# Kernel optimization log

Hardware: AMD Instinct MI355X
Metric: run time of the kernel (lower is better)

The kernel has to match this reference:

```python
import jax, jax.numpy as jnp
import numpy as np

D_MODEL = 1024
NUM_HEADS = 16
HEAD_DIM = D_MODEL // NUM_HEADS
THETA = 10000.0


def apply_rope(x, token_positions):
    # x: [B, H, S, d_head]; token_positions: [S] int
    d = x.shape[-1]
    inv_freq = THETA ** (-jnp.arange(0, d, 2, dtype=jnp.float32) / d)  # [d/2]
    ang = token_positions.astype(jnp.float32)[:, None] * inv_freq      # [S, d/2]
    cos, sin = jnp.cos(ang), jnp.sin(ang)
    x1 = x[..., 0::2]
    x2 = x[..., 1::2]
    out_even = x1 * cos - x2 * sin
    out_odd = x1 * sin + x2 * cos
    # interleave even/odd back: [..., S, d/2, 2] -> [..., S, d]
    return jnp.stack([out_even, out_odd], axis=-1).reshape(x.shape)


def setup_inputs() -> dict:
    key = jax.random.key(0)
    ks = jax.random.split(key, 5)
    scale = 1.0 / np.sqrt(D_MODEL)
    x = jax.random.normal(ks[0], (4, 2048, D_MODEL), dtype=jnp.float32)
    wq = jax.random.normal(ks[1], (D_MODEL, D_MODEL), dtype=jnp.float32) * scale
    wk = jax.random.normal(ks[2], (D_MODEL, D_MODEL), dtype=jnp.float32) * scale
    wv = jax.random.normal(ks[3], (D_MODEL, D_MODEL), dtype=jnp.float32) * scale
    wo = jax.random.normal(ks[4], (D_MODEL, D_MODEL), dtype=jnp.float32) * scale
    token_positions = jnp.arange(2048, dtype=jnp.int32)
    return {"x": x, "wq": wq, "wk": wk, "wv": wv, "wo": wo,
            "token_positions": token_positions}


def reference(x, wq, wk, wv, wo, token_positions):
    B, S, D = x.shape
    H, dh = NUM_HEADS, HEAD_DIM
    # fused QKV projection (Linear stores weight [out, in]; y = x @ W.T)
    q = jnp.einsum('bsd,ed->bse', x, wq).reshape(B, S, H, dh).transpose(0, 2, 1, 3)
    k = jnp.einsum('bsd,ed->bse', x, wk).reshape(B, S, H, dh).transpose(0, 2, 1, 3)
    v = jnp.einsum('bsd,ed->bse', x, wv).reshape(B, S, H, dh).transpose(0, 2, 1, 3)
    q = apply_rope(q, token_positions)
    k = apply_rope(k, token_positions)
    scores = jnp.einsum('bhid,bhjd->bhij', q, k) / jnp.sqrt(jnp.float32(dh))
    causal = jnp.tril(jnp.ones((S, S), dtype=bool))
    scores = jnp.where(causal, scores, -jnp.inf)
    attn = jax.nn.softmax(scores, axis=-1)
    out = jnp.einsum('bhij,bhjd->bhid', attn, v)            # [B,H,S,dh]
    out = out.transpose(0, 2, 1, 3).reshape(B, S, D)         # [B,S,D]
    return jnp.einsum('bsd,ed->bse', out, wo)
```

## Files before the change

### kernel.cpp

```cpp
#include <hip/hip_runtime.h>
#include <cstdint>
#include <cstddef>

typedef short bf16x8 __attribute__((ext_vector_type(8)));
typedef float f32x4 __attribute__((ext_vector_type(4)));
typedef unsigned short u16;
typedef u16 u16x4v __attribute__((ext_vector_type(4)));
typedef uint32_t u32x4v __attribute__((ext_vector_type(4)));

#define SEQ 2048
#define QSCALE 0.18033688011112042f
#define DEFER_THR 11.5415603f

static __device__ __forceinline__ u16 f2bf(float f) {
  uint32_t u = __builtin_bit_cast(uint32_t, f);
  u += 0x7fffu + ((u >> 16) & 1u);
  return (u16)(u >> 16);
}

static __device__ __forceinline__ uint32_t cvtpk_bf16(float lo, float hi) {
  uint32_t r;
  asm("v_cvt_pk_bf16_f32 %0, %1, %2" : "=v"(r) : "v"(lo), "v"(hi));
  return r;
}

#define MFMA_BF16(a, b, c) __builtin_amdgcn_mfma_f32_16x16x32_bf16((a), (b), (c), 0, 0, 0)

static __device__ __forceinline__ void gload_lds16(const void* g, void* l) {
  __builtin_amdgcn_global_load_lds((const __attribute__((address_space(1))) void*)g,
                                   (__attribute__((address_space(3))) void*)l, 16, 0, 0);
}

__global__ __launch_bounds__(256) void cvt_kernel(
    const float4* __restrict__ x, const float4* __restrict__ wq,
    const float4* __restrict__ wk, const float4* __restrict__ wv,
    const float4* __restrict__ wo, u16x4v* __restrict__ xb,
    u16x4v* __restrict__ wqkvb, u16x4v* __restrict__ wob) {
  const int id = blockIdx.x * 256 + threadIdx.x;
  const float4* src;
  u16x4v* dst;
  if (id < 2097152) { src = x + id; dst = xb + id; }
  else if (id < 2359296) {
    const int j = id - 2097152; const int e = j >> 8;
    const int ep = (e & ~63) | ((e & 63) >> 1) | ((e & 1) << 5);
    src = wq + j; dst = wqkvb + ep * 256 + (j & 255);
  } else if (id < 2621440) {
    const int j = id - 2359296; const int e = j >> 8;
    const int ep = (e & ~63) | ((e & 63) >> 1) | ((e & 1) << 5);
    src = wk + j; dst = wqkvb + 262144 + ep * 256 + (j & 255);
  } else if (id < 2883584) { const int j = id - 2621440; src = wv + j; dst = wqkvb + 524288 + j; }
  else { const int j = id - 2883584; src = wo + j; dst = wob + j; }
  const float4 v = *src;
  u16x4v o;
  o[0] = f2bf(v.x); o[1] = f2bf(v.y); o[2] = f2bf(v.z); o[3] = f2bf(v.w);
  *dst = o;
}

__global__ __launch_bounds__(256) void rope_tbl_kernel(const int* __restrict__ tp,
                                                       float2* __restrict__ tbl) {
  const int id = blockIdx.x * 256 + threadIdx.x;
  const int s = id >> 5, i = id & 31;
  const float pos = (float)tp[s];
  const float freq = powf(10000.0f, -(float)(2 * i) / 64.0f);
  const float ang = pos * freq;
  float sv, cv;
  sincosf(ang, &sv, &cv);
  tbl[id] = make_float2(cv, sv);
}

template <int MODE>
__global__ __launch_bounds__(256) void gemm_bt(const u16* __restrict__ A,
                                               const u16* __restrict__ Bt,
                                               void* __restrict__ Cout,
                                               u16* __restrict__ Vt,
                                               const float2* __restrict__ tbl,
                                               int M, int N, int K) {
  __shared__ __align__(16) u16 As[128 * 64];
  __shared__ __align__(16) u16 Bs[128 * 64];
  const int tid = threadIdx.x;
  const int w = tid >> 6;
  const int l = tid & 63;
  const int g = l >> 4;
  const int lr = l & 15;
  const int wm = (w >> 1) * 64;
  const int wn = (w & 1) * 64;
  const long tile_m = (long)blockIdx.y * 128;
  const long tile_n = (long)blockIdx.x * 128;

  const int lrow = l >> 3;
  const int lcolsw = (l & 7) ^ lrow;

  f32x4 acc[4][4] = {};

  for (int k0 = 0; k0 < K; k0 += 64) {
#pragma unroll
    for (int cc = 0; cc < 4; ++cc) {
      const int c = w * 4 + cc;
      const int row = c * 8 + lrow;
      gload_lds16(A + (tile_m + row) * (long)K + k0 + lcolsw * 8, As + c * 512);
      gload_lds16(Bt + (tile_n + row) * (long)K + k0 + lcolsw * 8, Bs + c * 512);
    }
    __syncthreads();
#pragma unroll
    for (int kk = 0; kk < 2; ++kk) {
      bf16x8 af[4], bfr[4];
#pragma unroll
      for (int mi = 0; mi < 4; ++mi) {
        const int row = wm + mi * 16 + lr;
        const int cc = ((kk << 2) + g) ^ (row & 7);
        af[mi] = *(const bf16x8*)((const char*)As + row * 128 + cc * 16);
      }
#pragma unroll
      for (int ni = 0; ni < 4; ++ni) {
        const int row = wn + ni * 16 + lr;
        const int cc = ((kk << 2) + g) ^ (row & 7);
        bfr[ni] = *(const bf16x8*)((const char*)Bs + row * 128 + cc * 16);
      }
#pragma unroll
      for (int mi = 0; mi < 4; ++mi)
#pragma unroll
        for (int ni = 0; ni < 4; ++ni)
          acc[mi][ni] = MFMA_BF16(af[mi], bfr[ni], acc[mi][ni]);
    }
    __syncthreads();
  }

  if constexpr (MODE == 0) {
    float* C = (float*)Cout;
#pragma unroll
    for (int mi = 0; mi < 4; ++mi) {
#pragma unroll
      for (int ni = 0; ni < 4; ++ni) {
        const long row0 = tile_m + wm + mi * 16 + g * 4;
        const long col = tile_n + wn + ni * 16 + lr;
#pragma unroll
        for (int r = 0; r < 4; ++r) C[(row0 + r) * N + col] = acc[mi][ni][r];
      }
    }
  } else {
    u16* C = (u16*)Cout;
    if (tile_n < 2048) {
      const float scale = (tile_n < 1024) ? QSCALE : 1.0f;
#pragma unroll
      for (int mi = 0; mi < 4; ++mi) {
        const long row0 = tile_m + wm + mi * 16 + g * 4;
#pragma unroll
        for (int np = 0; np < 2; ++np) {
          const long col = tile_n + wn + np * 16 + lr;
          const int i = (int)col & 31;
#pragma unroll
          for (int r = 0; r < 4; ++r) {
            const long row = row0 + r;
            const float2 cs = tbl[((int)row & (SEQ - 1)) * 32 + i];
            const float x1 = acc[mi][np][r];
            const float x2 = acc[mi][np + 2][r];
            C[row * N + col]      = f2bf((x1 * cs.x - x2 * cs.y) * scale);
            C[row * N + col + 32] = f2bf((x1 * cs.y + x2 * cs.x) * scale);
          }
        }
      }
    } else {
#pragma unroll
      for (int mi = 0; mi < 4; ++mi) {
        const long row0 = tile_m + wm + mi * 16 + g * 4;
        const int bb = (int)(row0 >> 11);
        const int s0 = (int)row0 & (SEQ - 1);
#pragma unroll
        for (int ni = 0; ni < 4; ++ni) {
          const int hd = (int)(tile_n + wn + ni * 16 + lr) - 2048;
          u16x4v pk;
#pragma unroll
          for (int r = 0; r < 4; ++r) pk[r] = f2bf(acc[mi][ni][r]);
          *(u16x4v*)(Vt + ((size_t)(bb * 16 + (hd >> 6)) * 64 + (hd & 63)) * SEQ + s0) = pk;
        }
      }
    }
  }
}

__global__ __launch_bounds__(256, 2) void attn_kernel(const u16* __restrict__ qkvb,
                                                      const u16* __restrict__ Vt,
                                                      u16* __restrict__ attn_out) {
  const int tid = threadIdx.x;
  const int w = tid >> 6;
  const int l = tid & 63;
  const int g = l >> 4;
  const int lr = l & 15;
  const int job = blockIdx.x;
  const int qt = 15 - (job >> 6);
  const int bh = job & 63;
  const int b = bh >> 4;
  const int h = bh & 15;

  const u16* Qb = qkvb + (size_t)b * SEQ * 3072 + h * 64;
  const u16* Kb = Qb + 1024;
  const u16* Vb = Vt + (size_t)bh * 64 * SEQ;

  const int krow0 = ((lr >> 2) << 3) + (lr & 3);

  const int wqb = qt * 128 + w * 32;

  bf16x8 qf[2][2];
#pragma unroll
  for (int s = 0; s < 2; ++s)
#pragma unroll
    for (int hf = 0; hf < 2; ++hf)
      qf[s][hf] = *(const bf16x8*)(Qb + (size_t)(wqb + s * 16 + lr) * 3072 + hf * 32 + g * 8);

  f32x4 O[2][4] = {};
  float m_s[2] = {-1e38f, -1e38f};
  float l_s[2] = {0.f, 0.f};

  const int n32 = (wqb >> 5) + 1;
  const int n64 = (n32 + 1) >> 1;

  bf16x8 kf[4][2];
#pragma unroll
  for (int X = 0; X < 4; ++X)
#pragma unroll
    for (int hf = 0; hf < 2; ++hf)
      kf[X][hf] = *(const bf16x8*)(Kb + (size_t)((X >> 1) * 32 + krow0 + (X & 1) * 4) * 3072 + hf * 32 + g * 8);

  for (int kt = 0; kt < n64; ++kt) {
    const int kbase = kt * 64;
    bf16x8 kn[4][2];
    {
      const int nb = kbase + 64;
#pragma unroll
      for (int X = 0; X < 4; ++X)
#pragma unroll
        for (int hf = 0; hf < 2; ++hf)
          kn[X][hf] = *(const bf16x8*)(Kb + (size_t)(nb + (X >> 1) * 32 + krow0 + (X & 1) * 4) * 3072 + hf * 32 + g * 8);
    }
    bf16x8 vf[4][2];
#pragma unroll
    for (int dt = 0; dt < 4; ++dt)
#pragma unroll
      for (int hv = 0; hv < 2; ++hv)
        vf[dt][hv] = *(const bf16x8*)(Vb + (size_t)(dt * 16 + lr) * SEQ + kbase + hv * 32 + g * 8);

    const bool diag = (kt == n64 - 1);
#pragma unroll
    for (int s = 0; s < 2; ++s) {
      f32x4 c[4] = {};
#pragma unroll
      for (int X = 0; X < 4; ++X) {
        c[X] = MFMA_BF16(kf[X][0], qf[s][0], c[X]);
        c[X] = MFMA_BF16(kf[X][1], qf[s][1], c[X]);
      }
      const int q = wqb + s * 16 + lr;
      float t[16];
#pragma unroll
      for (int X = 0; X < 4; ++X)
#pragma unroll
        for (int r = 0; r < 4; ++r) {
          float v = c[X][r];
          if (diag) {
            const int kk = kbase + (X >> 1) * 32 + g * 8 + (X & 1) * 4 + r;
            if (kk > q) v = -1e30f;
          }
          t[X * 4 + r] = v;
        }
      float m01 = fmaxf(t[0], t[1]), m23 = fmaxf(t[2], t[3]);
      float m45 = fmaxf(t[4], t[5]), m67 = fmaxf(t[6], t[7]);
      float m89 = fmaxf(t[8], t[9]), mab = fmaxf(t[10], t[11]);
      float mcd = fmaxf(t[12], t[13]), mef = fmaxf(t[14], t[15]);
      float pm = fmaxf(fmaxf(fmaxf(m01, m23), fmaxf(m45, m67)),
                       fmaxf(fmaxf(m89, mab), fmaxf(mcd, mef)));
      pm = fmaxf(pm, __shfl_xor(pm, 16));
      pm = fmaxf(pm, __shfl_xor(pm, 32));
      if (!__all(pm <= m_s[s] + DEFER_THR)) {
        const float mnew = fmaxf(m_s[s], pm);
        const float corr = __builtin_amdgcn_exp2f(m_s[s] - mnew);
        l_s[s] *= corr;
#pragma unroll
        for (int dt = 0; dt < 4; ++dt)
#pragma unroll
          for (int r = 0; r < 4; ++r) O[s][dt][r] *= corr;
        m_s[s] = mnew;
      }
      float p[16];
      float psum = 0.f;
#pragma unroll
      for (int i = 0; i < 16; ++i) {
        p[i] = __builtin_amdgcn_exp2f(t[i] - m_s[s]);
        psum += p[i];
      }
      psum += __shfl_xor(psum, 16);
      psum += __shfl_xor(psum, 32);
      l_s[s] += psum;

      u32x4v pk0, pk1;
#pragma unroll
      for (int j = 0; j < 4; ++j) {
        pk0[j] = cvtpk_bf16(p[2 * j], p[2 * j + 1]);
        pk1[j] = cvtpk_bf16(p[8 + 2 * j], p[8 + 2 * j + 1]);
      }
      const bf16x8 pf0 = __builtin_bit_cast(bf16x8, pk0);
      const bf16x8 pf1 = __builtin_bit_cast(bf16x8, pk1);
#pragma unroll
      for (int dt = 0; dt < 4; ++dt) {
        O[s][dt] = MFMA_BF16(vf[dt][0], pf0, O[s][dt]);
        O[s][dt] = MFMA_BF16(vf[dt][1], pf1, O[s][dt]);
      }
    }
#pragma unroll
    for (int X = 0; X < 4; ++X)
#pragma unroll
      for (int hf = 0; hf < 2; ++hf) kf[X][hf] = kn[X][hf];
  }

#pragma unroll
  for (int s = 0; s < 2; ++s) {
    const float inv = 1.0f / l_s[s];
    const int q = wqb + s * 16 + lr;
    u16* orow = attn_out + ((size_t)b * SEQ + q) * 1024 + h * 64;
#pragma unroll
    for (int dt = 0; dt < 4; ++dt) {
      u16x4v pk;
#pragma unroll
      for (int r = 0; r < 4; ++r) pk[r] = f2bf(O[s][dt][r] * inv);
      *(u16x4v*)(orow + dt * 16 + g * 4) = pk;
    }
  }
}

extern "C" void kernel_launch(void* const* d_in, const int* in_sizes, int n_in,
                              void* d_out, int out_size, void* d_ws, size_t ws_size,
                              hipStream_t stream) {
  const float* x = (const float*)d_in[0];
  const float* wq = (const float*)d_in[1];
  const float* wk = (const float*)d_in[2];
  const float* wv = (const float*)d_in[3];
  const float* wo = (const float*)d_in[4];
  const int* tp = (const int*)d_in[5];

  char* ws = (char*)d_ws;
  u16* xb       = (u16*)(ws + 0);
  u16* wqkvb    = (u16*)(ws + 16777216);
  u16* wob      = (u16*)(ws + 23068672);
  u16* qkvb     = (u16*)(ws + 25165824);
  u16* Vt       = (u16*)(ws + 75497472);
  u16* attn_out = (u16*)(ws + 92274688);
  float2* tbl   = (float2*)(ws + 109051904);

  cvt_kernel<<<12288, 256, 0, stream>>>((const float4*)x, (const float4*)wq,
                                        (const float4*)wk, (const float4*)wv,
                                        (const float4*)wo, (u16x4v*)xb,
                                        (u16x4v*)wqkvb, (u16x4v*)wob);
  rope_tbl_kernel<<<256, 256, 0, stream>>>(tp, tbl);
  gemm_bt<1><<<dim3(24, 64), 256, 0, stream>>>(xb, wqkvb, qkvb, Vt, tbl, 8192, 3072, 1024);
  attn_kernel<<<1024, 256, 0, stream>>>(qkvb, Vt, attn_out);
  gemm_bt<0><<<dim3(8, 64), 256, 0, stream>>>(attn_out, wob, d_out, nullptr, nullptr, 8192, 1024, 1024);
}
```

Before: 327.6 us.

## Balance causal attention work by pairing mirrored query groups per wave

```diff
diff --git a/kernel.cpp b/kernel.cpp
--- a/kernel.cpp
+++ b/kernel.cpp
@@ -178,7 +178,7 @@
   }
 }
 
-__global__ __launch_bounds__(256, 2) void attn_kernel(const u16* __restrict__ qkvb,
+__global__ __launch_bounds__(256, 4) void attn_kernel(const u16* __restrict__ qkvb,
                                                       const u16* __restrict__ Vt,
                                                       u16* __restrict__ attn_out) {
   const int tid = threadIdx.x;
@@ -187,8 +187,8 @@
   const int g = l >> 4;
   const int lr = l & 15;
   const int job = blockIdx.x;
-  const int qt = 15 - (job >> 6);
   const int bh = job & 63;
+  const int pr = (job >> 6) * 4 + w;
   const int b = bh >> 4;
   const int h = bh & 15;
 
@@ -198,97 +198,88 @@
 
   const int krow0 = ((lr >> 2) << 3) + (lr & 3);
 
-  const int wqb = qt * 128 + w * 32;
-
-  bf16x8 qf[2][2];
-#pragma unroll
-  for (int s = 0; s < 2; ++s)
+#pragma unroll
+  for (int half = 0; half < 2; ++half) {
+    const int qg = half ? pr : (127 - pr);
+    const int qrow = qg * 16 + lr;
+
+    bf16x8 qf[2];
 #pragma unroll
     for (int hf = 0; hf < 2; ++hf)
-      qf[s][hf] = *(const bf16x8*)(Qb + (size_t)(wqb + s * 16 + lr) * 3072 + hf * 32 + g * 8);
-
-  f32x4 O[2][4] = {};
-  float m_s[2] = {-1e38f, -1e38f};
-  float l_s[2] = {0.f, 0.f};
-
-  const int n32 = (wqb >> 5) + 1;
-  const int n64 = (n32 + 1) >> 1;
-
-  bf16x8 kf[4][2];
-#pragma unroll
-  for (int X = 0; X < 4; ++X)
-#pragma unroll
-    for (int hf = 0; hf < 2; ++hf)
-      kf[X][hf] = *(const bf16x8*)(Kb + (size_t)((X >> 1) * 32 + krow0 + (X & 1) * 4) * 3072 + hf * 32 + g * 8);
-
-  for (int kt = 0; kt < n64; ++kt) {
-    const int kbase = kt * 64;
-    bf16x8 kn[4][2];
-    {
-      const int nb = kbase + 64;
-#pragma unroll
-      for (int X = 0; X < 4; ++X)
-#pragma unroll
-        for (int hf = 0; hf < 2; ++hf)
-          kn[X][hf] = *(const bf16x8*)(Kb + (size_t)(nb + (X >> 1) * 32 + krow0 + (X & 1) * 4) * 3072 + hf * 32 + g * 8);
-    }
-    bf16x8 vf[4][2];
-#pragma unroll
-    for (int dt = 0; dt < 4; ++dt)
-#pragma unroll
-      for (int hv = 0; hv < 2; ++hv)
-        vf[dt][hv] = *(const bf16x8*)(Vb + (size_t)(dt * 16 + lr) * SEQ + kbase + hv * 32 + g * 8);
-
-    const bool diag = (kt == n64 - 1);
-#pragma unroll
-    for (int s = 0; s < 2; ++s) {
+      qf[hf] = *(const bf16x8*)(Qb + (size_t)qrow * 3072 + hf * 32 + g * 8);
+
+    f32x4 O[4] = {};
+    float m_s = -1e38f;
+    float l_s = 0.f;
+
+    const int n64 = (qg >> 2) + 1;
+
+    bf16x8 kf[4][2];
+#pragma unroll
+    for (int X = 0; X < 4; ++X)
+#pragma unroll
+      for (int hf = 0; hf < 2; ++hf)
+        kf[X][hf] = *(const bf16x8*)(Kb + (size_t)((X >> 1) * 32 + krow0 + (X & 1) * 4) * 3072 + hf * 32 + g * 8);
+
+    for (int kt = 0; kt < n64; ++kt) {
+      const int kbase = kt * 64;
+      bf16x8 kn[4][2];
+      {
+        const int nb = kbase + 64;
+#pragma unroll
+        for (int X = 0; X < 4; ++X)
+#pragma unroll
+          for (int hf = 0; hf < 2; ++hf)
+            kn[X][hf] = *(const bf16x8*)(Kb + (size_t)(nb + (X >> 1) * 32 + krow0 + (X & 1) * 4) * 3072 + hf * 32 + g * 8);
+      }
+      bf16x8 vf[4][2];
+#pragma unroll
+      for (int dt = 0; dt < 4; ++dt)
+#pragma unroll
+        for (int hv = 0; hv < 2; ++hv)
+          vf[dt][hv] = *(const bf16x8*)(Vb + (size_t)(dt * 16 + lr) * SEQ + kbase + hv * 32 + g * 8);
+
       f32x4 c[4] = {};
 #pragma unroll
       for (int X = 0; X < 4; ++X) {
-        c[X] = MFMA_BF16(kf[X][0], qf[s][0], c[X]);
-        c[X] = MFMA_BF16(kf[X][1], qf[s][1], c[X]);
-      }
-      const int q = wqb + s * 16 + lr;
-      float t[16];
-#pragma unroll
-      for (int X = 0; X < 4; ++X)
-#pragma unroll
-        for (int r = 0; r < 4; ++r) {
-          float v = c[X][r];
-          if (diag) {
+        c[X] = MFMA_BF16(kf[X][0], qf[0], c[X]);
+        c[X] = MFMA_BF16(kf[X][1], qf[1], c[X]);
+      }
+      if (kt == n64 - 1) {
+#pragma unroll
+        for (int X = 0; X < 4; ++X)
+#pragma unroll
+          for (int r = 0; r < 4; ++r) {
             const int kk = kbase + (X >> 1) * 32 + g * 8 + (X & 1) * 4 + r;
-            if (kk > q) v = -1e30f;
+            if (kk > qrow) c[X][r] = -1e30f;
           }
-          t[X * 4 + r] = v;
-        }
-      float m01 = fmaxf(t[0], t[1]), m23 = fmaxf(t[2], t[3]);
-      float m45 = fmaxf(t[4], t[5]), m67 = fmaxf(t[6], t[7]);
-      float m89 = fmaxf(t[8], t[9]), mab = fmaxf(t[10], t[11]);
-      float mcd = fmaxf(t[12], t[13]), mef = fmaxf(t[14], t[15]);
-      float pm = fmaxf(fmaxf(fmaxf(m01, m23), fmaxf(m45, m67)),
-                       fmaxf(fmaxf(m89, mab), fmaxf(mcd, mef)));
+      }
+      float m0 = fmaxf(fmaxf(c[0][0], c[0][1]), fmaxf(c[0][2], c[0][3]));
+      float m1 = fmaxf(fmaxf(c[1][0], c[1][1]), fmaxf(c[1][2], c[1][3]));
+      float m2 = fmaxf(fmaxf(c[2][0], c[2][1]), fmaxf(c[2][2], c[2][3]));
+      float m3 = fmaxf(fmaxf(c[3][0], c[3][1]), fmaxf(c[3][2], c[3][3]));
+      float pm = fmaxf(fmaxf(m0, m1), fmaxf(m2, m3));
       pm = fmaxf(pm, __shfl_xor(pm, 16));
       pm = fmaxf(pm, __shfl_xor(pm, 32));
-      if (!__all(pm <= m_s[s] + DEFER_THR)) {
-        const float mnew = fmaxf(m_s[s], pm);
-        const float corr = __builtin_amdgcn_exp2f(m_s[s] - mnew);
-        l_s[s] *= corr;
+      if (!__all(pm <= m_s + DEFER_THR)) {
+        const float mnew = fmaxf(m_s, pm);
+        const float corr = __builtin_amdgcn_exp2f(m_s - mnew);
+        l_s *= corr;
 #pragma unroll
         for (int dt = 0; dt < 4; ++dt)
 #pragma unroll
-          for (int r = 0; r < 4; ++r) O[s][dt][r] *= corr;
-        m_s[s] = mnew;
+          for (int r = 0; r < 4; ++r) O[dt][r] *= corr;
+        m_s = mnew;
       }
       float p[16];
-      float psum = 0.f;
-#pragma unroll
-      for (int i = 0; i < 16; ++i) {
-        p[i] = __builtin_amdgcn_exp2f(t[i] - m_s[s]);
-        psum += p[i];
-      }
-      psum += __shfl_xor(psum, 16);
-      psum += __shfl_xor(psum, 32);
-      l_s[s] += psum;
+#pragma unroll
+      for (int X = 0; X < 4; ++X)
+#pragma unroll
+        for (int r = 0; r < 4; ++r) {
+          const float e = __builtin_amdgcn_exp2f(c[X][r] - m_s);
+          p[X * 4 + r] = e;
+          l_s += e;
+        }
 
       u32x4v pk0, pk1;
 #pragma unroll
@@ -300,26 +291,24 @@
       const bf16x8 pf1 = __builtin_bit_cast(bf16x8, pk1);
 #pragma unroll
       for (int dt = 0; dt < 4; ++dt) {
-        O[s][dt] = MFMA_BF16(vf[dt][0], pf0, O[s][dt]);
-        O[s][dt] = MFMA_BF16(vf[dt][1], pf1, O[s][dt]);
-      }
-    }
-#pragma unroll
-    for (int X = 0; X < 4; ++X)
-#pragma unroll
-      for (int hf = 0; hf < 2; ++hf) kf[X][hf] = kn[X][hf];
-  }
-
-#pragma unroll
-  for (int s = 0; s < 2; ++s) {
-    const float inv = 1.0f / l_s[s];
-    const int q = wqb + s * 16 + lr;
-    u16* orow = attn_out + ((size_t)b * SEQ + q) * 1024 + h * 64;
+        O[dt] = MFMA_BF16(vf[dt][0], pf0, O[dt]);
+        O[dt] = MFMA_BF16(vf[dt][1], pf1, O[dt]);
+      }
+#pragma unroll
+      for (int X = 0; X < 4; ++X)
+#pragma unroll
+        for (int hf = 0; hf < 2; ++hf) kf[X][hf] = kn[X][hf];
+    }
+
+    l_s += __shfl_xor(l_s, 16);
+    l_s += __shfl_xor(l_s, 32);
+    const float inv = 1.0f / l_s;
+    u16* orow = attn_out + ((size_t)b * SEQ + qrow) * 1024 + h * 64;
 #pragma unroll
     for (int dt = 0; dt < 4; ++dt) {
       u16x4v pk;
 #pragma unroll
-      for (int r = 0; r < 4; ++r) pk[r] = f2bf(O[s][dt][r] * inv);
+      for (int r = 0; r < 4; ++r) pk[r] = f2bf(O[dt][r] * inv);
       *(u16x4v*)(orow + dt * 16 + g * 4) = pk;
     }
   }
```

Result: slower. 445.6 us (+36.0%).
